# Optimization experiments

Measured on AMD Instinct MI355X. Metric: run time of the kernel, lower is better.

## Reference

```python
import jax, jax.numpy as jnp
import numpy as np

USER_NUM = 100000
ITEM_NUM = 50000
E = 128   # embedding_size
A = 64    # attention_size
M = 8     # memory_size
B = 4096  # batch
NF = 50   # friends per user


def _l2norm(x, axis):
    # torch F.normalize(p=2): x / max(||x||, eps)
    n = jnp.sqrt(jnp.sum(x * x, axis=axis, keepdims=True))
    return x / jnp.maximum(n, 1e-12)


def setup_inputs() -> dict:
    key = jax.random.key(0)
    ks = jax.random.split(key, 9)
    u = lambda k, shape: jax.random.uniform(k, shape, jnp.float32, -0.1, 0.1)
    return {
        "input_u": jax.random.randint(ks[0], (B,), 0, USER_NUM),
        "input_i": jax.random.randint(ks[1], (B,), 0, ITEM_NUM),
        "input_uf": jax.random.randint(ks[2], (B, NF), 0, USER_NUM + 1),
        "uidW": u(ks[3], (USER_NUM + 1, E)),
        "iidW": u(ks[4], (ITEM_NUM, E)),
        "i_bias": jnp.zeros((ITEM_NUM,), jnp.float32),
        "Key": u(ks[5], (E, M)),
        "Mem": jnp.ones((M, E), jnp.float32),
        "WA": u(ks[6], (E, A)),
        "BA": jnp.zeros((A,), jnp.float32),
        "U_omega": u(ks[7], (A, 1)),
    }


def reference(input_u, input_i, input_uf, uidW, iidW, i_bias, Key, Mem, WA, BA, U_omega):
    user_num = uidW.shape[0] - 1  # padding id
    uid = uidW[input_u]                      # [B, E]
    iid = iidW[input_i]                      # [B, E]
    i_b = i_bias[input_i]                    # [B]
    fe = uidW[input_uf]                      # [B, F, E] friend embeddings
    fn = (input_uf != user_num).astype(uid.dtype)  # [B, F] valid-friend mask

    fe = fn[:, :, None] * fe
    uid_n = _l2norm(uid, axis=1)
    fe_n = _l2norm(fe, axis=2)
    cross = uid_n[:, None, :] * fe_n                     # [B, F, E]
    att_key = jnp.einsum('bfe,em->bfm', cross, Key)      # [B, F, M]
    att_mem = jax.nn.softmax(att_key, axis=0)            # softmax over batch (faithful to dim=0)
    att_mem = fn[:, :, None] * att_mem
    f1 = jnp.einsum('bfm,me->bfe', att_mem, Mem)         # [B, F, E]
    f2 = f1 * fe
    h = jax.nn.relu(jnp.einsum('bfe,ea->bfa', f2, WA) + BA)
    j = jnp.exp(jnp.einsum('bfa,ao->bfo', h, U_omega))   # [B, F, 1]
    j = fn[:, :, None] * j
    w = j / (jnp.sum(j, axis=1, keepdims=True) + 1e-8)
    friend = jnp.sum(w * f2, axis=1)                     # [B, E] (dropout p=0 -> identity)
    user = uid + friend
    score = jnp.sum(user * iid, axis=1) + i_b            # [B]
    return score
```

## Files before the change

### kernel.cpp

```cpp
#include <hip/hip_runtime.h>

#define EDIM 128
#define MDIM 8
#define ADIM 64
#define NFR  50
#define NCOL (NFR * MDIM)

typedef __attribute__((ext_vector_type(8))) short short8;
typedef __attribute__((ext_vector_type(4))) float f32x4;

__device__ __forceinline__ float waveReduceSum(float v) {
    #pragma unroll
    for (int s = 32; s >= 1; s >>= 1) v += __shfl_xor(v, s, 64);
    return v;
}
__device__ __forceinline__ short f2bf(float x) {
    unsigned u = __float_as_uint(x);
    u += 0x7FFFu + ((u >> 16) & 1u);
    return (short)(u >> 16);
}
__device__ __forceinline__ float bf2f(short s) {
    return __uint_as_float(((unsigned)(unsigned short)s) << 16);
}
__device__ __forceinline__ int fragOff(int r, int e) {
    int q = (e >> 3) & 3;
    int slot = (q * 16 + (r & 15)) ^ (q << 1);
    int block = ((r >> 4) << 2) | (e >> 5);
    return (block * 64 + slot) * 8;
}
__device__ __forceinline__ int slotR(int l) { return l ^ (((l >> 4) & 3) << 1); }

__global__ __launch_bounds__(256)
void k0_prep(const float* __restrict__ WA, const float* __restrict__ Key,
             short* __restrict__ WAfrag, short* __restrict__ Keyfrag)
{
    int t = blockIdx.x * 256 + threadIdx.x;
    if (t < 1024) {
        int lane = t & 63;
        int Kt = (t >> 6) & 3;
        int Nt = t >> 8;
        int n  = Nt * 16 + (lane & 15);
        int k0 = Kt * 32 + (lane >> 4) * 8;
        short8 v;
        #pragma unroll
        for (int j = 0; j < 8; ++j) v[j] = f2bf(WA[(size_t)(k0 + j) * ADIM + n]);
        *(short8*)(WAfrag + (size_t)t * 8) = v;
    } else if (t < 1280) {
        int i = t - 1024;
        int lane = i & 63;
        int Kt = i >> 6;
        int n  = lane & 15;
        int k0 = Kt * 32 + (lane >> 4) * 8;
        short8 v;
        #pragma unroll
        for (int j = 0; j < 8; ++j)
            v[j] = (n < MDIM) ? f2bf(Key[(size_t)(k0 + j) * MDIM + n]) : (short)0;
        *(short8*)(Keyfrag + (size_t)i * 8) = v;
    }
}

__global__ __launch_bounds__(256, 4)
void k1_attkey(const int* __restrict__ input_u, const int* __restrict__ input_uf,
               const float* __restrict__ uidW, const short* __restrict__ Keyfrag,
               float* __restrict__ att_key, int user_num)
{
    const int b = blockIdx.x, t = threadIdx.x, w = t >> 6, l = t & 63;
    __shared__ short crossF[64 * EDIM];
    __shared__ float uidnL[EDIM];
    __shared__ float redW[4];
    __shared__ int ufL[64];

    const int u = input_u[b];
    float x = (t < EDIM) ? uidW[(size_t)u * EDIM + t] : 0.f;
    float s = waveReduceSum(x * x);
    if (l == 0) redW[w] = s;
    if (t < NFR) ufL[t] = input_uf[(size_t)b * NFR + t];
    else if (t < 64) ufL[t] = user_num;
    __syncthreads();
    float uinv = 1.0f / fmaxf(sqrtf(redW[0] + redW[1] + redW[2] + redW[3]), 1e-12f);
    if (t < EDIM) uidnL[t] = x * uinv;
    __syncthreads();

    const int kg = t & 15, fl = t >> 4;
    const int e0 = kg * 8;
    float4 un0 = *(const float4*)&uidnL[e0];
    float4 un1 = *(const float4*)&uidnL[e0 + 4];

    #pragma unroll
    for (int it = 0; it < 4; ++it) {
        int f = fl + 16 * it;
        short8 outv = {0, 0, 0, 0, 0, 0, 0, 0};
        if (f < NFR) {
            int fid = ufL[f];
            float fn = (fid != user_num) ? 1.f : 0.f;
            const float* fp = uidW + (size_t)fid * EDIM + e0;
            float4 g0 = *(const float4*)fp;
            float4 g1 = *(const float4*)(fp + 4);
            g0.x *= fn; g0.y *= fn; g0.z *= fn; g0.w *= fn;
            g1.x *= fn; g1.y *= fn; g1.z *= fn; g1.w *= fn;
            float fss = g0.x*g0.x + g0.y*g0.y + g0.z*g0.z + g0.w*g0.w
                      + g1.x*g1.x + g1.y*g1.y + g1.z*g1.z + g1.w*g1.w;
            fss += __shfl_xor(fss, 1, 64);
            fss += __shfl_xor(fss, 2, 64);
            fss += __shfl_xor(fss, 4, 64);
            fss += __shfl_xor(fss, 8, 64);
            float inv = 1.0f / fmaxf(sqrtf(fss), 1e-12f);
            outv[0] = f2bf(un0.x * g0.x * inv);
            outv[1] = f2bf(un0.y * g0.y * inv);
            outv[2] = f2bf(un0.z * g0.z * inv);
            outv[3] = f2bf(un0.w * g0.w * inv);
            outv[4] = f2bf(un1.x * g1.x * inv);
            outv[5] = f2bf(un1.y * g1.y * inv);
            outv[6] = f2bf(un1.z * g1.z * inv);
            outv[7] = f2bf(un1.w * g1.w * inv);
        }
        *(short8*)&crossF[fragOff(f, e0)] = outv;
    }
    __syncthreads();

    f32x4 acc = {0.f, 0.f, 0.f, 0.f};
    const int sl = slotR(l);
    #pragma unroll
    for (int Kt = 0; Kt < 4; ++Kt) {
        short8 a  = *(const short8*)&crossF[(((w << 2) | Kt) * 64 + sl) * 8];
        short8 bf = *(const short8*)(Keyfrag + (size_t)((Kt * 64 + l)) * 8);
        acc = __builtin_amdgcn_mfma_f32_16x16x32_bf16(a, bf, acc, 0, 0, 0);
    }
    const int m = l & 15;
    if (m < MDIM) {
        const int fbase = w * 16 + (l >> 4) * 4;
        #pragma unroll
        for (int r = 0; r < 4; ++r) {
            int f = fbase + r;
            if (f < NFR) att_key[((size_t)b * NFR + f) * MDIM + m] = acc[r];
        }
    }
}

__global__ __launch_bounds__(256)
void k2a_stats(const float* __restrict__ ak,
               float* __restrict__ Pm, float* __restrict__ Ps, int B)
{
    const int cg = blockIdx.x;
    const int rc = blockIdx.y;
    const int t = threadIdx.x;
    const int c = t & 15, r = t >> 4;
    const int col = cg * 16 + c;
    const int base = rc * (B >> 4);

    float x[16];
    #pragma unroll
    for (int k = 0; k < 16; ++k)
        x[k] = ak[(size_t)(base + k * 16 + r) * NCOL + col];
    float m = x[0];
    #pragma unroll
    for (int k = 1; k < 16; ++k) m = fmaxf(m, x[k]);
    float s = 0.f;
    #pragma unroll
    for (int k = 0; k < 16; ++k) s += __expf(x[k] - m);

    __shared__ float mL[16][17], sL[16][17];
    mL[r][c] = m; sL[r][c] = s;
    __syncthreads();
    if (t < 16) {
        float M = mL[0][t];
        #pragma unroll
        for (int rr = 1; rr < 16; ++rr) M = fmaxf(M, mL[rr][t]);
        float S = 0.f;
        #pragma unroll
        for (int rr = 0; rr < 16; ++rr) S += sL[rr][t] * __expf(mL[rr][t] - M);
        Pm[rc * NCOL + cg * 16 + t] = M;
        Ps[rc * NCOL + cg * 16 + t] = S;
    }
}

__global__ __launch_bounds__(512)
void k2b_merge(const float* __restrict__ Pm, const float* __restrict__ Ps,
               float* __restrict__ mx, float* __restrict__ ise)
{
    int col = threadIdx.x;
    if (col >= NCOL) return;
    float M = -3.4e38f;
    #pragma unroll
    for (int rc = 0; rc < 16; ++rc) M = fmaxf(M, Pm[rc * NCOL + col]);
    float S = 0.f;
    #pragma unroll
    for (int rc = 0; rc < 16; ++rc) S += Ps[rc * NCOL + col] * __expf(Pm[rc * NCOL + col] - M);
    mx[col] = M;
    ise[col] = 1.0f / S;
}

__global__ __launch_bounds__(256, 4)
void k3_final(const int* __restrict__ input_u, const int* __restrict__ input_i,
              const int* __restrict__ input_uf, const float* __restrict__ uidW,
              const float* __restrict__ iidW, const float* __restrict__ i_bias,
              const float* __restrict__ Mem, const short* __restrict__ WAfrag,
              const float* __restrict__ BA, const float* __restrict__ U_omega,
              const float* __restrict__ att_key, const float* __restrict__ mx,
              const float* __restrict__ ise, float* __restrict__ out,
              int user_num)
{
    const int b = blockIdx.x, t = threadIdx.x, w = t >> 6, l = t & 63;
    __shared__ short f2F[64 * EDIM];
    __shared__ float amL[NCOL];
    __shared__ int ufL[64];
    __shared__ float pPart[4 * 64];
    __shared__ float jxL[64];
    __shared__ float accW[4][EDIM];
    __shared__ float red2[2];
    __shared__ float wsS;

    if (t < NFR) ufL[t] = input_uf[(size_t)b * NFR + t];
    else if (t < 64) ufL[t] = user_num;
    __syncthreads();

    for (int i = t; i < NCOL; i += 256) {
        float ak = att_key[(size_t)b * NCOL + i];
        amL[i] = (ufL[i >> 3] != user_num) ? __expf(ak - mx[i]) * ise[i] : 0.f;
    }

    const int kg = t & 15, fl = t >> 4;
    const int e0 = kg * 8;
    float4 mA[MDIM], mB[MDIM];
    #pragma unroll
    for (int m = 0; m < MDIM; ++m) {
        mA[m] = *(const float4*)&Mem[m * EDIM + e0];
        mB[m] = *(const float4*)&Mem[m * EDIM + e0 + 4];
    }
    __syncthreads();

    #pragma unroll
    for (int it = 0; it < 4; ++it) {
        int f = fl + 16 * it;
        short8 outv = {0, 0, 0, 0, 0, 0, 0, 0};
        if (f < NFR) {
            int fid = ufL[f];
            float fn = (fid != user_num) ? 1.f : 0.f;
            const float* fp = uidW + (size_t)fid * EDIM + e0;
            float4 g0 = *(const float4*)fp;
            float4 g1 = *(const float4*)(fp + 4);
            float4 am0 = *(const float4*)&amL[f * 8];
            float4 am1 = *(const float4*)&amL[f * 8 + 4];
            float4 fa = {0.f, 0.f, 0.f, 0.f}, fb = {0.f, 0.f, 0.f, 0.f};
            #pragma unroll
            for (int m = 0; m < 4; ++m) {
                float c0 = (&am0.x)[m], c1 = (&am1.x)[m];
                fa.x += c0 * mA[m].x + c1 * mA[m + 4].x;
                fa.y += c0 * mA[m].y + c1 * mA[m + 4].y;
                fa.z += c0 * mA[m].z + c1 * mA[m + 4].z;
                fa.w += c0 * mA[m].w + c1 * mA[m + 4].w;
                fb.x += c0 * mB[m].x + c1 * mB[m + 4].x;
                fb.y += c0 * mB[m].y + c1 * mB[m + 4].y;
                fb.z += c0 * mB[m].z + c1 * mB[m + 4].z;
                fb.w += c0 * mB[m].w + c1 * mB[m + 4].w;
            }
            outv[0] = f2bf(fa.x * g0.x * fn);
            outv[1] = f2bf(fa.y * g0.y * fn);
            outv[2] = f2bf(fa.z * g0.z * fn);
            outv[3] = f2bf(fa.w * g0.w * fn);
            outv[4] = f2bf(fb.x * g1.x * fn);
            outv[5] = f2bf(fb.y * g1.y * fn);
            outv[6] = f2bf(fb.z * g1.z * fn);
            outv[7] = f2bf(fb.w * g1.w * fn);
        }
        *(short8*)&f2F[fragOff(f, e0)] = outv;
    }
    __syncthreads();

    const int sl = slotR(l);
    f32x4 acc[4];
    #pragma unroll
    for (int Mt = 0; Mt < 4; ++Mt) acc[Mt] = (f32x4){0.f, 0.f, 0.f, 0.f};
    #pragma unroll
    for (int Kt = 0; Kt < 4; ++Kt) {
        short8 bf = *(const short8*)(WAfrag + (size_t)(((w << 2) | Kt) * 64 + l) * 8);
        #pragma unroll
        for (int Mt = 0; Mt < 4; ++Mt) {
            short8 a = *(const short8*)&f2F[(((Mt << 2) | Kt) * 64 + sl) * 8];
            acc[Mt] = __builtin_amdgcn_mfma_f32_16x16x32_bf16(a, bf, acc[Mt], 0, 0, 0);
        }
    }

    const int aIdx = w * 16 + (l & 15);
    const float ba = BA[aIdx];
    const float uo = U_omega[aIdx];
    float v[16];
    #pragma unroll
    for (int Mt = 0; Mt < 4; ++Mt)
        #pragma unroll
        for (int r = 0; r < 4; ++r)
            v[Mt * 4 + r] = fmaxf(acc[Mt][r] + ba, 0.f) * uo;

    const bool c0 = l & 1, c1 = l & 2, c2 = l & 4, c3 = l & 8;
    #pragma unroll
    for (int k = 0; k < 8; ++k) {
        float lo = v[k], hi = v[k + 8];
        float send = c0 ? lo : hi;
        float recv = __shfl_xor(send, 1, 64);
        v[k] = c0 ? (hi + recv) : (lo + recv);
    }
    #pragma unroll
    for (int k = 0; k < 4; ++k) {
        float lo = v[k], hi = v[k + 4];
        float send = c1 ? lo : hi;
        float recv = __shfl_xor(send, 2, 64);
        v[k] = c1 ? (hi + recv) : (lo + recv);
    }
    #pragma unroll
    for (int k = 0; k < 2; ++k) {
        float lo = v[k], hi = v[k + 2];
        float send = c2 ? lo : hi;
        float recv = __shfl_xor(send, 4, 64);
        v[k] = c2 ? (hi + recv) : (lo + recv);
    }
    {
        float lo = v[0], hi = v[1];
        float send = c3 ? lo : hi;
        float recv = __shfl_xor(send, 8, 64);
        v[0] = c3 ? (hi + recv) : (lo + recv);
    }
    const int vIdx = ((l & 1) << 3) | ((l & 2) << 1) | ((l & 4) >> 1) | ((l & 8) >> 3);
    const int fLane = (vIdx >> 2) * 16 + (l >> 4) * 4 + (vIdx & 3);
    pPart[w * 64 + fLane] = v[0];
    __syncthreads();

    if (t < 64) {
        float p = pPart[t] + pPart[64 + t] + pPart[128 + t] + pPart[192 + t];
        float jv = 0.f;
        if (t < NFR && ufL[t] != user_num) jv = __expf(p);
        jxL[t] = jv;
        float wsum = waveReduceSum(jv);
        if (t == 0) wsS = wsum + 1e-8f;
    }
    __syncthreads();

    float pa[8] = {0.f, 0.f, 0.f, 0.f, 0.f, 0.f, 0.f, 0.f};
    #pragma unroll
    for (int it = 0; it < 4; ++it) {
        int f = fl + 16 * it;
        float jf = jxL[f];
        short8 vv = *(const short8*)&f2F[fragOff(f, e0)];
        #pragma unroll
        for (int j = 0; j < 8; ++j) pa[j] += jf * bf2f(vv[j]);
    }
    #pragma unroll
    for (int j = 0; j < 8; ++j) {
        pa[j] += __shfl_xor(pa[j], 16, 64);
        pa[j] += __shfl_xor(pa[j], 32, 64);
    }
    if (l < 16) {
        #pragma unroll
        for (int j = 0; j < 8; ++j) accW[w][l * 8 + j] = pa[j];
    }
    __syncthreads();

    if (t < EDIM) {
        const float winv = 1.0f / wsS;
        float fr = (accW[0][t] + accW[1][t] + accW[2][t] + accW[3][t]) * winv;
        const int u = input_u[b];
        const int ii = input_i[b];
        float sc = (uidW[(size_t)u * EDIM + t] + fr) * iidW[(size_t)ii * EDIM + t];
        float p = waveReduceSum(sc);
        if ((t & 63) == 0) red2[t >> 6] = p;
    }
    __syncthreads();
    if (t == 0) out[b] = red2[0] + red2[1] + i_bias[input_i[b]];
}

extern "C" void kernel_launch(void* const* d_in, const int* in_sizes, int n_in,
                              void* d_out, int out_size, void* d_ws, size_t ws_size,
                              hipStream_t stream)
{
    const int*   input_u  = (const int*)d_in[0];
    const int*   input_i  = (const int*)d_in[1];
    const int*   input_uf = (const int*)d_in[2];
    const float* uidW     = (const float*)d_in[3];
    const float* iidW     = (const float*)d_in[4];
    const float* i_bias   = (const float*)d_in[5];
    const float* Key      = (const float*)d_in[6];
    const float* Mem      = (const float*)d_in[7];
    const float* WA       = (const float*)d_in[8];
    const float* BA       = (const float*)d_in[9];
    const float* U_om     = (const float*)d_in[10];

    const int B = in_sizes[0];
    const int user_num = in_sizes[3] / EDIM - 1;

    float* att = (float*)d_ws;
    float* Pm  = att + (size_t)B * NCOL;
    float* Ps  = Pm + 16 * NCOL;
    float* mx  = Ps + 16 * NCOL;
    float* ise = mx + NCOL;
    short* WAfrag  = (short*)(ise + NCOL);
    short* Keyfrag = WAfrag + 4 * 4 * 64 * 8;

    k0_prep<<<5, 256, 0, stream>>>(WA, Key, WAfrag, Keyfrag);
    k1_attkey<<<B, 256, 0, stream>>>(input_u, input_uf, uidW, Keyfrag, att, user_num);
    k2a_stats<<<dim3(25, 16), 256, 0, stream>>>(att, Pm, Ps, B);
    k2b_merge<<<1, 512, 0, stream>>>(Pm, Ps, mx, ise);
    k3_final<<<B, 256, 0, stream>>>(input_u, input_i, input_uf, uidW, iidW, i_bias,
                                    Mem, WAfrag, BA, U_om, att, mx, ise,
                                    (float*)d_out, user_num);
}
```

Measured before the change: 172.9 us.

## Fuse softmax column sums into attkey via sliced atomics and cache bf16 friend embeddings

Removes the separate stats kernel. Each attkey block now atomically adds exp(att_key) into one of 64 slice buffers, and a small merge kernel sums the slices. Softmax max-subtraction is dropped, which relies on att_key being small because the inputs are normalized and the Key values are bounded. The attkey kernel also writes the masked friend embeddings as bf16 to a workspace, so the final kernel reads that compact copy instead of re-gathering from the fp32 table. The cost is atomic contention and the extra bf16 write and read traffic.

```diff
diff --git a/kernel.cpp b/kernel.cpp
--- a/kernel.cpp
+++ b/kernel.cpp
@@ -5,6 +5,7 @@
 #define ADIM 64
 #define NFR  50
 #define NCOL (NFR * MDIM)
+#define NSLICE 64
 
 typedef __attribute__((ext_vector_type(8))) short short8;
 typedef __attribute__((ext_vector_type(4))) float f32x4;
@@ -32,9 +33,11 @@
 
 __global__ __launch_bounds__(256)
 void k0_prep(const float* __restrict__ WA, const float* __restrict__ Key,
-             short* __restrict__ WAfrag, short* __restrict__ Keyfrag)
+             short* __restrict__ WAfrag, short* __restrict__ Keyfrag,
+             float* __restrict__ Ssum)
 {
     int t = blockIdx.x * 256 + threadIdx.x;
+    for (int i = t; i < NSLICE * NCOL; i += 5 * 256) Ssum[i] = 0.f;
     if (t < 1024) {
         int lane = t & 63;
         int Kt = (t >> 6) & 3;
@@ -62,7 +65,8 @@
 __global__ __launch_bounds__(256, 4)
 void k1_attkey(const int* __restrict__ input_u, const int* __restrict__ input_uf,
                const float* __restrict__ uidW, const short* __restrict__ Keyfrag,
-               float* __restrict__ att_key, int user_num)
+               float* __restrict__ att_key, short* __restrict__ feW,
+               float* __restrict__ Ssum, int user_num)
 {
     const int b = blockIdx.x, t = threadIdx.x, w = t >> 6, l = t & 63;
     __shared__ short crossF[64 * EDIM];
@@ -98,6 +102,12 @@
             float4 g1 = *(const float4*)(fp + 4);
             g0.x *= fn; g0.y *= fn; g0.z *= fn; g0.w *= fn;
             g1.x *= fn; g1.y *= fn; g1.z *= fn; g1.w *= fn;
+            short8 fev;
+            fev[0] = f2bf(g0.x); fev[1] = f2bf(g0.y);
+            fev[2] = f2bf(g0.z); fev[3] = f2bf(g0.w);
+            fev[4] = f2bf(g1.x); fev[5] = f2bf(g1.y);
+            fev[6] = f2bf(g1.z); fev[7] = f2bf(g1.w);
+            *(short8*)(feW + ((size_t)b * NFR + f) * EDIM + e0) = fev;
             float fss = g0.x*g0.x + g0.y*g0.y + g0.z*g0.z + g0.w*g0.w
                       + g1.x*g1.x + g1.y*g1.y + g1.z*g1.z + g1.w*g1.w;
             fss += __shfl_xor(fss, 1, 64);
@@ -128,65 +138,27 @@
     }
     const int m = l & 15;
     if (m < MDIM) {
+        float* Ss = Ssum + (size_t)(b & (NSLICE - 1)) * NCOL;
         const int fbase = w * 16 + (l >> 4) * 4;
         #pragma unroll
         for (int r = 0; r < 4; ++r) {
             int f = fbase + r;
-            if (f < NFR) att_key[((size_t)b * NFR + f) * MDIM + m] = acc[r];
+            if (f < NFR) {
+                att_key[((size_t)b * NFR + f) * MDIM + m] = acc[r];
+                atomicAdd(&Ss[f * MDIM + m], __expf(acc[r]));
+            }
         }
     }
 }
 
 __global__ __launch_bounds__(256)
-void k2a_stats(const float* __restrict__ ak,
-               float* __restrict__ Pm, float* __restrict__ Ps, int B)
-{
-    const int cg = blockIdx.x;
-    const int rc = blockIdx.y;
-    const int t = threadIdx.x;
-    const int c = t & 15, r = t >> 4;
-    const int col = cg * 16 + c;
-    const int base = rc * (B >> 4);
-
-    float x[16];
-    #pragma unroll
-    for (int k = 0; k < 16; ++k)
-        x[k] = ak[(size_t)(base + k * 16 + r) * NCOL + col];
-    float m = x[0];
-    #pragma unroll
-    for (int k = 1; k < 16; ++k) m = fmaxf(m, x[k]);
-    float s = 0.f;
-    #pragma unroll
-    for (int k = 0; k < 16; ++k) s += __expf(x[k] - m);
-
-    __shared__ float mL[16][17], sL[16][17];
-    mL[r][c] = m; sL[r][c] = s;
-    __syncthreads();
-    if (t < 16) {
-        float M = mL[0][t];
-        #pragma unroll
-        for (int rr = 1; rr < 16; ++rr) M = fmaxf(M, mL[rr][t]);
-        float S = 0.f;
-        #pragma unroll
-        for (int rr = 0; rr < 16; ++rr) S += sL[rr][t] * __expf(mL[rr][t] - M);
-        Pm[rc * NCOL + cg * 16 + t] = M;
-        Ps[rc * NCOL + cg * 16 + t] = S;
-    }
-}
-
-__global__ __launch_bounds__(512)
-void k2b_merge(const float* __restrict__ Pm, const float* __restrict__ Ps,
-               float* __restrict__ mx, float* __restrict__ ise)
-{
-    int col = threadIdx.x;
+void k2b_merge(const float* __restrict__ Ssum, float* __restrict__ ise)
+{
+    int col = blockIdx.x * 256 + threadIdx.x;
     if (col >= NCOL) return;
-    float M = -3.4e38f;
-    #pragma unroll
-    for (int rc = 0; rc < 16; ++rc) M = fmaxf(M, Pm[rc * NCOL + col]);
     float S = 0.f;
     #pragma unroll
-    for (int rc = 0; rc < 16; ++rc) S += Ps[rc * NCOL + col] * __expf(Pm[rc * NCOL + col] - M);
-    mx[col] = M;
+    for (int s = 0; s < NSLICE; ++s) S += Ssum[s * NCOL + col];
     ise[col] = 1.0f / S;
 }
 
@@ -196,7 +168,7 @@
               const float* __restrict__ iidW, const float* __restrict__ i_bias,
               const float* __restrict__ Mem, const short* __restrict__ WAfrag,
               const float* __restrict__ BA, const float* __restrict__ U_omega,
-              const float* __restrict__ att_key, const float* __restrict__ mx,
+              const float* __restrict__ att_key, const short* __restrict__ feW,
               const float* __restrict__ ise, float* __restrict__ out,
               int user_num)
 {
@@ -216,7 +188,7 @@
 
     for (int i = t; i < NCOL; i += 256) {
         float ak = att_key[(size_t)b * NCOL + i];
-        amL[i] = (ufL[i >> 3] != user_num) ? __expf(ak - mx[i]) * ise[i] : 0.f;
+        amL[i] = (ufL[i >> 3] != user_num) ? __expf(ak) * ise[i] : 0.f;
     }
 
     const int kg = t & 15, fl = t >> 4;
@@ -234,11 +206,7 @@
         int f = fl + 16 * it;
         short8 outv = {0, 0, 0, 0, 0, 0, 0, 0};
         if (f < NFR) {
-            int fid = ufL[f];
-            float fn = (fid != user_num) ? 1.f : 0.f;
-            const float* fp = uidW + (size_t)fid * EDIM + e0;
-            float4 g0 = *(const float4*)fp;
-            float4 g1 = *(const float4*)(fp + 4);
+            short8 fv = *(const short8*)(feW + ((size_t)b * NFR + f) * EDIM + e0);
             float4 am0 = *(const float4*)&amL[f * 8];
             float4 am1 = *(const float4*)&amL[f * 8 + 4];
             float4 fa = {0.f, 0.f, 0.f, 0.f}, fb = {0.f, 0.f, 0.f, 0.f};
@@ -254,14 +222,14 @@
                 fb.z += c0 * mB[m].z + c1 * mB[m + 4].z;
                 fb.w += c0 * mB[m].w + c1 * mB[m + 4].w;
             }
-            outv[0] = f2bf(fa.x * g0.x * fn);
-            outv[1] = f2bf(fa.y * g0.y * fn);
-            outv[2] = f2bf(fa.z * g0.z * fn);
-            outv[3] = f2bf(fa.w * g0.w * fn);
-            outv[4] = f2bf(fb.x * g1.x * fn);
-            outv[5] = f2bf(fb.y * g1.y * fn);
-            outv[6] = f2bf(fb.z * g1.z * fn);
-            outv[7] = f2bf(fb.w * g1.w * fn);
+            outv[0] = f2bf(fa.x * bf2f(fv[0]));
+            outv[1] = f2bf(fa.y * bf2f(fv[1]));
+            outv[2] = f2bf(fa.z * bf2f(fv[2]));
+            outv[3] = f2bf(fa.w * bf2f(fv[3]));
+            outv[4] = f2bf(fb.x * bf2f(fv[4]));
+            outv[5] = f2bf(fb.y * bf2f(fv[5]));
+            outv[6] = f2bf(fb.z * bf2f(fv[6]));
+            outv[7] = f2bf(fb.w * bf2f(fv[7]));
         }
         *(short8*)&f2F[fragOff(f, e0)] = outv;
     }
@@ -386,19 +354,18 @@
     const int B = in_sizes[0];
     const int user_num = in_sizes[3] / EDIM - 1;
 
-    float* att = (float*)d_ws;
-    float* Pm  = att + (size_t)B * NCOL;
-    float* Ps  = Pm + 16 * NCOL;
-    float* mx  = Ps + 16 * NCOL;
-    float* ise = mx + NCOL;
+    float* att  = (float*)d_ws;
+    float* Ssum = att + (size_t)B * NCOL;
+    float* ise  = Ssum + NSLICE * NCOL;
     short* WAfrag  = (short*)(ise + NCOL);
     short* Keyfrag = WAfrag + 4 * 4 * 64 * 8;
-
-    k0_prep<<<5, 256, 0, stream>>>(WA, Key, WAfrag, Keyfrag);
-    k1_attkey<<<B, 256, 0, stream>>>(input_u, input_uf, uidW, Keyfrag, att, user_num);
-    k2a_stats<<<dim3(25, 16), 256, 0, stream>>>(att, Pm, Ps, B);
-    k2b_merge<<<1, 512, 0, stream>>>(Pm, Ps, mx, ise);
+    short* feW     = Keyfrag + 4 * 64 * 8;
+
+    k0_prep<<<5, 256, 0, stream>>>(WA, Key, WAfrag, Keyfrag, Ssum);
+    k1_attkey<<<B, 256, 0, stream>>>(input_u, input_uf, uidW, Keyfrag, att, feW,
+                                     Ssum, user_num);
+    k2b_merge<<<2, 256, 0, stream>>>(Ssum, ise);
     k3_final<<<B, 256, 0, stream>>>(input_u, input_i, input_uf, uidW, iidW, i_bias,
-                                    Mem, WAfrag, BA, U_om, att, mx, ise,
+                                    Mem, WAfrag, BA, U_om, att, feW, ise,
                                     (float*)d_out, user_num);
 }
```

New measurement: 187.1 us. 1.08x slower.
